# Performance work log

Hardware: AMD Instinct MI355X
Metric: run time of the kernel (lower is better)

The kernel has to match this reference:

```python
import jax, jax.numpy as jnp
import numpy as np

N = 25000   # nodes
E = 400000  # edges
F_IN = 128  # in_features
F_E = 16    # edge_features
C = 32      # channel_width
F_OUT = 1   # out_features
SLOPE = 0.01  # torch LeakyReLU default negative_slope


def leaky_relu(x):
    return jnp.where(x >= 0, x, SLOPE * x)


def setup_inputs() -> dict:
    key = jax.random.key(0)
    ks = jax.random.split(key, 12)
    x = jax.random.normal(ks[0], (N, F_IN), dtype=jnp.float32)
    edge_index = jax.random.randint(ks[1], (2, E), 0, N, dtype=jnp.int64)
    edge_attr = jax.random.normal(ks[2], (E, F_E), dtype=jnp.float32)
    # parameters (scaled like kaiming-ish fan-in init)
    W_in = jax.random.normal(ks[3], (F_IN, C), dtype=jnp.float32) / np.sqrt(F_IN)
    b_in = jnp.zeros((C,), dtype=jnp.float32)
    W_edge = jax.random.normal(ks[4], (F_E, C * C), dtype=jnp.float32) / np.sqrt(F_E)
    b_edge = jnp.zeros((C * C,), dtype=jnp.float32)
    W_root = jax.random.normal(ks[5], (C, C), dtype=jnp.float32) / np.sqrt(C)
    b_conv = jnp.zeros((C,), dtype=jnp.float32)
    W_out = jax.random.normal(ks[6], (C, F_OUT), dtype=jnp.float32) / np.sqrt(C)
    b_out = jnp.zeros((F_OUT,), dtype=jnp.float32)
    return {
        "x": x, "edge_index": edge_index, "edge_attr": edge_attr,
        "W_in": W_in, "b_in": b_in, "W_edge": W_edge, "b_edge": b_edge,
        "W_root": W_root, "b_conv": b_conv, "W_out": W_out, "b_out": b_out,
    }


def reference(x, edge_index, edge_attr, W_in, b_in, W_edge, b_edge,
              W_root, b_conv, W_out, b_out):
    # input projection (dropout = identity in eval mode)
    h = leaky_relu(x @ W_in + b_in)                       # [N, C]

    # NNConv layer (gnn_depth = 1):
    # per-edge weight matrix from edge_nn: Linear + LeakyReLU
    We = leaky_relu(edge_attr @ W_edge + b_edge)          # [E, C*C]
    We = We.reshape(E, C, C)                              # [E, C, C]
    src, dst = edge_index[0], edge_index[1]               # PyG: j=source, i=target
    # gather source node features, per-edge matvec, scatter-add to targets
    msg = jnp.einsum('ec,eco->eo', h[src], We)            # [E, C]
    aggr = jax.ops.segment_sum(msg, dst, num_segments=N)  # [N, C]
    h = aggr + h @ W_root + b_conv                        # root weight + bias
    h = leaky_relu(h)

    return h @ W_out + b_out                              # [N, F_OUT]
```

## Files before the change

### kernel.cpp

```cpp
#include <hip/hip_runtime.h>

#define NN 25000
#define EE 400000
#define FIN 128
#define FE 16
#define CH 32
#define SLOPE 0.01f
#define PROJ_BLOCKS 391
#define AUX_BLOCKS 32
#define WROW 24
#define WTP_SHORTS (1024 * WROW)
#define NTILES (EE / 128)
#define PBLK 1024

typedef __attribute__((ext_vector_type(8))) short bf16x8;
typedef __attribute__((ext_vector_type(4))) float f32x4;

__device__ __forceinline__ float lrelu(float v) { return fmaxf(v, SLOPE * v); }

__device__ __forceinline__ f32x4 lrelu4(f32x4 v) {
    f32x4 s = v * SLOPE;
#if __has_builtin(__builtin_elementwise_max)
    return __builtin_elementwise_max(v, s);
#else
    f32x4 r;
    r[0] = fmaxf(v[0], s[0]); r[1] = fmaxf(v[1], s[1]);
    r[2] = fmaxf(v[2], s[2]); r[3] = fmaxf(v[3], s[3]);
    return r;
#endif
}

__device__ __forceinline__ short f2bf(float f) {
    union { float f; unsigned u; } v; v.f = f;
    unsigned r = (v.u + 0x7fffu + ((v.u >> 16) & 1u)) >> 16;
    return (short)r;
}

__global__ void __launch_bounds__(256)
k_pre(const float* __restrict__ x, const float* __restrict__ W_in,
      const float* __restrict__ b_in, const float* __restrict__ W_edge,
      const float* __restrict__ b_edge,
      float* __restrict__ h, float* __restrict__ aggr, short* __restrict__ WtP) {
    __shared__ short Wt1[CH * 136];
    int tid = threadIdx.x;

    if (blockIdx.x >= PROJ_BLOCKS) {
        int ab = blockIdx.x - PROJ_BLOCKS;
        if (ab < 4) {
            int co = ab * 256 + tid;
            short row[WROW] __attribute__((aligned(16)));
#pragma unroll
            for (int k = 0; k < 16; k++) row[k] = f2bf(W_edge[k * 1024 + co]);
            row[16] = f2bf(b_edge[co]);
#pragma unroll
            for (int k = 17; k < WROW; k++) row[k] = 0;
            uint4* dstp = (uint4*)(WtP + co * WROW);
            int p0 = co % 3;
            int p1 = p0 + 1; if (p1 == 3) p1 = 0;
            int p2 = p1 + 1; if (p2 == 3) p2 = 0;
            dstp[p0] = ((uint4*)row)[0];
            dstp[p1] = ((uint4*)row)[1];
            dstp[p2] = ((uint4*)row)[2];
        } else {
            int t = (ab - 4) * 256 + tid;
            float4 z = make_float4(0.f, 0.f, 0.f, 0.f);
            for (int i = t; i < NN * CH / 4; i += (AUX_BLOCKS - 4) * 256)
                ((float4*)aggr)[i] = z;
        }
        return;
    }

#pragma unroll
    for (int i = 0; i < 16; i++) {
        int id = tid + 256 * i;
        int k = id >> 5, c = id & 31;
        Wt1[c * 136 + k] = f2bf(W_in[id]);
    }
    __syncthreads();

    int wave = tid >> 6, lane = tid & 63;
    int n16 = lane & 15, quad = lane >> 4;
    int node0 = blockIdx.x * 64 + wave * 16;

    f32x4 D[2];
#pragma unroll
    for (int ch = 0; ch < 2; ch++) {
        float bb = b_in[ch * 16 + n16];
        D[ch] = (f32x4){bb, bb, bb, bb};
    }
    int arow = node0 + n16; if (arow >= NN) arow = NN - 1;
#pragma unroll
    for (int kb = 0; kb < 4; kb++) {
        const float4* xp = (const float4*)(x + (size_t)arow * FIN + kb * 32 + quad * 8);
        float4 xa = xp[0], xb = xp[1];
        bf16x8 A = (bf16x8){f2bf(xa.x), f2bf(xa.y), f2bf(xa.z), f2bf(xa.w),
                            f2bf(xb.x), f2bf(xb.y), f2bf(xb.z), f2bf(xb.w)};
#pragma unroll
        for (int ch = 0; ch < 2; ch++) {
            bf16x8 B = *(const bf16x8*)&Wt1[(ch * 16 + n16) * 136 + kb * 32 + quad * 8];
            D[ch] = __builtin_amdgcn_mfma_f32_16x16x32_bf16(A, B, D[ch], 0, 0, 0);
        }
    }
#pragma unroll
    for (int ch = 0; ch < 2; ch++)
#pragma unroll
        for (int r = 0; r < 4; r++) {
            int nn = node0 + quad * 4 + r;
            if (nn < NN) h[(size_t)nn * CH + ch * 16 + n16] = lrelu(D[ch][r]);
        }
}

__global__ void __launch_bounds__(256, 2)
k_edge(const short* __restrict__ WtP,
       const float* __restrict__ ea,
       const int* __restrict__ src,
       const int* __restrict__ dst,
       const float* __restrict__ h,
       float* __restrict__ aggr) {
    __shared__ short WtL[WTP_SHORTS];
    __shared__ float hsT[2][CH * 128];

    int tid = threadIdx.x;

#pragma unroll
    for (int j = 0; j < 12; j++) {
        int idx = tid + 256 * j;
        ((uint4*)WtL)[idx] = ((const uint4*)WtP)[idx];
    }

    int eH = tid >> 1, halfH = tid & 1;
    int wave = tid >> 6, lane = tid & 63;
    int n16 = lane & 15, quad = lane >> 4;
    int t0 = wave * 32, t1 = t0 + 16;

    int s0 = (quad == 3) ? 0 : quad;
    int rot = (s0 + n16) % 3;
    const short* Bb[3];
#pragma unroll
    for (int j = 0; j < 3; j++) {
        int p = rot + j; if (p >= 3) p -= 3;
        Bb[j] = WtL + n16 * WROW + p * 8;
    }

    struct PrefT {
        float hv[16];
        float4 e0a, e0b, e1a, e1b;
        int d[8];
    };
    PrefT Pa, Pb;

    auto PREF = [&](int tile, PrefT& P) {
        int base = tile * 128;
        int s = src[base + eH];
        const float4* hp = (const float4*)(h + (size_t)s * CH + halfH * 16);
        float4 v0 = hp[0], v1 = hp[1], v2 = hp[2], v3 = hp[3];
        *(float4*)&P.hv[0] = v0;  *(float4*)&P.hv[4] = v1;
        *(float4*)&P.hv[8] = v2;  *(float4*)&P.hv[12] = v3;
        if (quad < 2) {
            const float4* p0 = (const float4*)(ea + (size_t)(base + t0 + n16) * FE + quad * 8);
            P.e0a = p0[0]; P.e0b = p0[1];
            const float4* p1 = (const float4*)(ea + (size_t)(base + t1 + n16) * FE + quad * 8);
            P.e1a = p1[0]; P.e1b = p1[1];
        }
#pragma unroll
        for (int r = 0; r < 4; r++) {
            P.d[r]     = dst[base + t0 + quad * 4 + r];
            P.d[4 + r] = dst[base + t1 + quad * 4 + r];
        }
    };

    auto WRITE = [&](float* hbuf, PrefT& P) {
        float* hd = hbuf + halfH * (16 * 128) + eH;
#pragma unroll
        for (int j = 0; j < 16; j++) hd[j * 128] = P.hv[j];
    };

    auto COMPUTE = [&](const float* hbuf, PrefT& P) {
        bf16x8 A0 = (bf16x8){0,0,0,0,0,0,0,0}, A1 = A0;
        if (quad < 2) {
            A0 = (bf16x8){f2bf(P.e0a.x), f2bf(P.e0a.y), f2bf(P.e0a.z), f2bf(P.e0a.w),
                          f2bf(P.e0b.x), f2bf(P.e0b.y), f2bf(P.e0b.z), f2bf(P.e0b.w)};
            A1 = (bf16x8){f2bf(P.e1a.x), f2bf(P.e1a.y), f2bf(P.e1a.z), f2bf(P.e1a.w),
                          f2bf(P.e1b.x), f2bf(P.e1b.y), f2bf(P.e1b.z), f2bf(P.e1b.w)};
        } else if (quad == 2) {
            A0[0] = (short)0x3F80; A1[0] = (short)0x3F80;
        }

        f32x4 m0[2], m1[2];
        m0[0] = (f32x4){0,0,0,0}; m0[1] = m0[0]; m1[0] = m0[0]; m1[1] = m0[0];
        const f32x4 Z = (f32x4){0,0,0,0};
        const float* h0b = hbuf + t0 + quad * 4;
        const float* h1b = hbuf + t1 + quad * 4;

#pragma unroll
        for (int c = 0; c < 32; c++) {
            f32x4 hc0 = *(const f32x4*)(h0b + c * 128);
            f32x4 hc1 = *(const f32x4*)(h1b + c * 128);
#pragma unroll
            for (int oh = 0; oh < 2; oh++) {
                int cb = c * 2 + oh;
                bf16x8 B = *(const bf16x8*)(Bb[cb % 3] + cb * (16 * WROW));
                f32x4 D0 = __builtin_amdgcn_mfma_f32_16x16x32_bf16(A0, B, Z, 0, 0, 0);
                f32x4 D1 = __builtin_amdgcn_mfma_f32_16x16x32_bf16(A1, B, Z, 0, 0, 0);
                m0[oh] += hc0 * lrelu4(D0);
                m1[oh] += hc1 * lrelu4(D1);
            }
        }

#pragma unroll
        for (int r = 0; r < 4; r++) {
#pragma unroll
            for (int oh = 0; oh < 2; oh++) {
                unsafeAtomicAdd(&aggr[(size_t)P.d[r]     * CH + oh * 16 + n16], m0[oh][r]);
                unsafeAtomicAdd(&aggr[(size_t)P.d[4 + r] * CH + oh * 16 + n16], m1[oh][r]);
            }
        }
    };

    int tile = blockIdx.x;
    PREF(tile, Pa);
    while (true) {
        WRITE(&hsT[0][0], Pa);
        __syncthreads();
        int nt = tile + PBLK;
        bool more = (nt < NTILES);
        if (more) PREF(nt, Pb);
        COMPUTE(&hsT[0][0], Pa);
        if (!more) break;
        tile = nt;

        WRITE(&hsT[1][0], Pb);
        __syncthreads();
        nt = tile + PBLK;
        more = (nt < NTILES);
        if (more) PREF(nt, Pa);
        COMPUTE(&hsT[1][0], Pb);
        if (!more) break;
        tile = nt;
    }
}

__global__ void __launch_bounds__(256)
k_node(const float* __restrict__ aggr,
       const float* __restrict__ h,
       const float* __restrict__ W_root,
       const float* __restrict__ b_conv,
       const float* __restrict__ W_out,
       const float* __restrict__ b_out,
       float* __restrict__ out) {
    __shared__ short WrB[CH * 40];
    __shared__ float WoS[CH];
    int tid = threadIdx.x;
    if (tid < 128) {
        int o = tid >> 2, c0 = (tid & 3) * 8;
        short tmp[8] __attribute__((aligned(16)));
#pragma unroll
        for (int j = 0; j < 8; j++) tmp[j] = f2bf(W_root[(c0 + j) * CH + o]);
        *(bf16x8*)&WrB[o * 40 + c0] = *(bf16x8*)tmp;
    } else if (tid < 160) {
        WoS[tid - 128] = W_out[tid - 128];
    }
    __syncthreads();

    int wave = tid >> 6, lane = tid & 63;
    int n16 = lane & 15, quad = lane >> 4;
    int node0 = blockIdx.x * 64 + wave * 16;

    int arow = node0 + n16; if (arow >= NN) arow = NN - 1;
    const float4* hp = (const float4*)(h + (size_t)arow * CH + quad * 8);
    float4 ha = hp[0], hb = hp[1];
    bf16x8 A = (bf16x8){f2bf(ha.x), f2bf(ha.y), f2bf(ha.z), f2bf(ha.w),
                        f2bf(hb.x), f2bf(hb.y), f2bf(hb.z), f2bf(hb.w)};
    float bc0 = b_conv[n16], bc1 = b_conv[16 + n16];
    f32x4 C0, C1;
#pragma unroll
    for (int r = 0; r < 4; r++) {
        int nr = node0 + quad * 4 + r; int cr = (nr < NN) ? nr : NN - 1;
        C0[r] = aggr[(size_t)cr * CH + n16] + bc0;
        C1[r] = aggr[(size_t)cr * CH + 16 + n16] + bc1;
    }
    bf16x8 B0 = *(const bf16x8*)&WrB[n16 * 40 + quad * 8];
    bf16x8 B1 = *(const bf16x8*)&WrB[(16 + n16) * 40 + quad * 8];
    f32x4 D0 = __builtin_amdgcn_mfma_f32_16x16x32_bf16(A, B0, C0, 0, 0, 0);
    f32x4 D1 = __builtin_amdgcn_mfma_f32_16x16x32_bf16(A, B1, C1, 0, 0, 0);

    float w0 = WoS[n16], w1 = WoS[16 + n16];
    f32x4 p;
#pragma unroll
    for (int r = 0; r < 4; r++)
        p[r] = lrelu(D0[r]) * w0 + lrelu(D1[r]) * w1;
#pragma unroll
    for (int mk = 1; mk < 16; mk <<= 1) {
#pragma unroll
        for (int r = 0; r < 4; r++) p[r] += __shfl_xor(p[r], mk, 64);
    }
    if (n16 == 0) {
        float bo = b_out[0];
#pragma unroll
        for (int r = 0; r < 4; r++) {
            int nr = node0 + quad * 4 + r;
            if (nr < NN) out[nr] = p[r] + bo;
        }
    }
}

extern "C" void kernel_launch(void* const* d_in, const int* in_sizes, int n_in,
                              void* d_out, int out_size, void* d_ws, size_t ws_size,
                              hipStream_t stream) {
    const float* x      = (const float*)d_in[0];
    const int*   ei     = (const int*)d_in[1];
    const float* ea     = (const float*)d_in[2];
    const float* W_in   = (const float*)d_in[3];
    const float* b_in   = (const float*)d_in[4];
    const float* W_edge = (const float*)d_in[5];
    const float* b_edge = (const float*)d_in[6];
    const float* W_root = (const float*)d_in[7];
    const float* b_conv = (const float*)d_in[8];
    const float* W_out  = (const float*)d_in[9];
    const float* b_out  = (const float*)d_in[10];
    float* out  = (float*)d_out;
    float* h    = (float*)d_ws;
    float* aggr = h + (size_t)NN * CH;
    short* WtP  = (short*)(aggr + (size_t)NN * CH);

    k_pre<<<PROJ_BLOCKS + AUX_BLOCKS, 256, 0, stream>>>(x, W_in, b_in, W_edge, b_edge,
                                                        h, aggr, WtP);
    k_edge<<<PBLK, 256, 0, stream>>>(WtP, ea, ei, ei + EE, h, aggr);
    k_node<<<PROJ_BLOCKS, 256, 0, stream>>>(aggr, h, W_root, b_conv, W_out, b_out, out);
}
```

Measured before the change: 163.6 us.

## Move edge bias to MFMA accumulator init and compact swizzled W_edge LDS layout

The edge-network bias no longer rides in the MFMA K dimension as a padded 24-short row with rotated placement. It is loaded as fp32 into LDS and fed in as the MFMA C accumulator. The bf16 weight table shrinks to 16 shorts per output with an XOR swizzle to avoid bank conflicts. This cuts LDS footprint, drops the three-way rotating pointer arithmetic, and keeps the bias in full precision. The h staging goes from double-buffered to a single buffer with an extra barrier, and the grid drops from 1024 to 768 blocks, which may cost some overlap between loads and compute.

```diff
diff --git a/kernel.cpp b/kernel.cpp
--- a/kernel.cpp
+++ b/kernel.cpp
@@ -8,10 +8,10 @@
 #define SLOPE 0.01f
 #define PROJ_BLOCKS 391
 #define AUX_BLOCKS 32
-#define WROW 24
-#define WTP_SHORTS (1024 * WROW)
-#define NTILES (EE / 128)
-#define PBLK 1024
+#define W16_SHORTS (1024 * 16)
+#define EPT 128
+#define NT (EE / EPT)
+#define PBLK 768
 
 typedef __attribute__((ext_vector_type(8))) short bf16x8;
 typedef __attribute__((ext_vector_type(4))) float f32x4;
@@ -36,11 +36,16 @@
     return (short)r;
 }
 
+__device__ __forceinline__ bf16x8 cvt8(const float4& a, const float4& b) {
+    return (bf16x8){f2bf(a.x), f2bf(a.y), f2bf(a.z), f2bf(a.w),
+                    f2bf(b.x), f2bf(b.y), f2bf(b.z), f2bf(b.w)};
+}
+
 __global__ void __launch_bounds__(256)
 k_pre(const float* __restrict__ x, const float* __restrict__ W_in,
       const float* __restrict__ b_in, const float* __restrict__ W_edge,
       const float* __restrict__ b_edge,
-      float* __restrict__ h, float* __restrict__ aggr, short* __restrict__ WtP) {
+      float* __restrict__ h, float* __restrict__ aggr, short* __restrict__ WtP16) {
     __shared__ short Wt1[CH * 136];
     int tid = threadIdx.x;
 
@@ -48,19 +53,11 @@
         int ab = blockIdx.x - PROJ_BLOCKS;
         if (ab < 4) {
             int co = ab * 256 + tid;
-            short row[WROW] __attribute__((aligned(16)));
+            short row[16] __attribute__((aligned(16)));
 #pragma unroll
             for (int k = 0; k < 16; k++) row[k] = f2bf(W_edge[k * 1024 + co]);
-            row[16] = f2bf(b_edge[co]);
-#pragma unroll
-            for (int k = 17; k < WROW; k++) row[k] = 0;
-            uint4* dstp = (uint4*)(WtP + co * WROW);
-            int p0 = co % 3;
-            int p1 = p0 + 1; if (p1 == 3) p1 = 0;
-            int p2 = p1 + 1; if (p2 == 3) p2 = 0;
-            dstp[p0] = ((uint4*)row)[0];
-            dstp[p1] = ((uint4*)row)[1];
-            dstp[p2] = ((uint4*)row)[2];
+            uint4* dstp = (uint4*)(WtP16 + co * 16);
+            dstp[0] = ((uint4*)row)[0]; dstp[1] = ((uint4*)row)[1];
         } else {
             int t = (ab - 4) * 256 + tid;
             float4 z = make_float4(0.f, 0.f, 0.f, 0.f);
@@ -93,8 +90,7 @@
     for (int kb = 0; kb < 4; kb++) {
         const float4* xp = (const float4*)(x + (size_t)arow * FIN + kb * 32 + quad * 8);
         float4 xa = xp[0], xb = xp[1];
-        bf16x8 A = (bf16x8){f2bf(xa.x), f2bf(xa.y), f2bf(xa.z), f2bf(xa.w),
-                            f2bf(xb.x), f2bf(xb.y), f2bf(xb.z), f2bf(xb.w)};
+        bf16x8 A = cvt8(xa, xb);
 #pragma unroll
         for (int ch = 0; ch < 2; ch++) {
             bf16x8 B = *(const bf16x8*)&Wt1[(ch * 16 + n16) * 136 + kb * 32 + quad * 8];
@@ -111,36 +107,41 @@
 }
 
 __global__ void __launch_bounds__(256, 2)
-k_edge(const short* __restrict__ WtP,
+k_edge(const short* __restrict__ WtP16,
        const float* __restrict__ ea,
        const int* __restrict__ src,
        const int* __restrict__ dst,
        const float* __restrict__ h,
-       float* __restrict__ aggr) {
-    __shared__ short WtL[WTP_SHORTS];
-    __shared__ float hsT[2][CH * 128];
+       float* __restrict__ aggr,
+       const float* __restrict__ b_edge) {
+    __shared__ short W16[W16_SHORTS];
+    __shared__ float biasF[1024];
+    __shared__ float hsT[CH * EPT];
 
     int tid = threadIdx.x;
 
 #pragma unroll
-    for (int j = 0; j < 12; j++) {
+    for (int j = 0; j < 9; j++) {
         int idx = tid + 256 * j;
-        ((uint4*)WtL)[idx] = ((const uint4*)WtP)[idx];
-    }
-
-    int eH = tid >> 1, halfH = tid & 1;
-    int wave = tid >> 6, lane = tid & 63;
-    int n16 = lane & 15, quad = lane >> 4;
-    int t0 = wave * 32, t1 = t0 + 16;
-
-    int s0 = (quad == 3) ? 0 : quad;
-    int rot = (s0 + n16) % 3;
-    const short* Bb[3];
-#pragma unroll
-    for (int j = 0; j < 3; j++) {
-        int p = rot + j; if (p >= 3) p -= 3;
-        Bb[j] = WtL + n16 * WROW + p * 8;
-    }
+        if (idx < 2048) {
+            int co = idx >> 1, s = idx & 1;
+            int p = (co << 1) | (s ^ ((co >> 2) & 1));
+            ((uint4*)W16)[p] = ((const uint4*)WtP16)[idx];
+        } else if (idx < 2304) {
+            ((uint4*)biasF)[idx - 2048] = ((const uint4*)b_edge)[idx - 2048];
+        }
+    }
+
+    const int lane = tid & 63;
+    const int wave = tid >> 6;
+    const int n16 = lane & 15, quad = lane >> 4;
+    const int t0 = wave * 32, t1 = t0 + 16;
+    const int eH = tid >> 1, halfH = tid & 1;
+
+    const int qeff = (quad & 1) ^ ((n16 >> 2) & 1);
+    const short* Bbase = W16 + n16 * 16 + qeff * 8;
+    const float* h0b = hsT + t0 + quad * 4;
+    const float* h1b = hsT + t1 + quad * 4;
 
     struct PrefT {
         float hv[16];
@@ -150,7 +151,7 @@
     PrefT Pa, Pb;
 
     auto PREF = [&](int tile, PrefT& P) {
-        int base = tile * 128;
+        int base = tile * EPT;
         int s = src[base + eH];
         const float4* hp = (const float4*)(h + (size_t)s * CH + halfH * 16);
         float4 v0 = hp[0], v1 = hp[1], v2 = hp[2], v3 = hp[3];
@@ -169,41 +170,40 @@
         }
     };
 
-    auto WRITE = [&](float* hbuf, PrefT& P) {
-        float* hd = hbuf + halfH * (16 * 128) + eH;
-#pragma unroll
-        for (int j = 0; j < 16; j++) hd[j * 128] = P.hv[j];
+    auto WRITE = [&](PrefT& P) {
+        float* hd = hsT + halfH * (16 * EPT) + eH;
+#pragma unroll
+        for (int j = 0; j < 16; j++) hd[j * EPT] = P.hv[j];
     };
 
-    auto COMPUTE = [&](const float* hbuf, PrefT& P) {
+    auto COMPUTE = [&](PrefT& P) {
         bf16x8 A0 = (bf16x8){0,0,0,0,0,0,0,0}, A1 = A0;
-        if (quad < 2) {
-            A0 = (bf16x8){f2bf(P.e0a.x), f2bf(P.e0a.y), f2bf(P.e0a.z), f2bf(P.e0a.w),
-                          f2bf(P.e0b.x), f2bf(P.e0b.y), f2bf(P.e0b.z), f2bf(P.e0b.w)};
-            A1 = (bf16x8){f2bf(P.e1a.x), f2bf(P.e1a.y), f2bf(P.e1a.z), f2bf(P.e1a.w),
-                          f2bf(P.e1b.x), f2bf(P.e1b.y), f2bf(P.e1b.z), f2bf(P.e1b.w)};
-        } else if (quad == 2) {
-            A0[0] = (short)0x3F80; A1[0] = (short)0x3F80;
-        }
+        if (quad < 2) { A0 = cvt8(P.e0a, P.e0b); A1 = cvt8(P.e1a, P.e1b); }
 
         f32x4 m0[2], m1[2];
         m0[0] = (f32x4){0,0,0,0}; m0[1] = m0[0]; m1[0] = m0[0]; m1[1] = m0[0];
-        const f32x4 Z = (f32x4){0,0,0,0};
-        const float* h0b = hbuf + t0 + quad * 4;
-        const float* h1b = hbuf + t1 + quad * 4;
 
 #pragma unroll
         for (int c = 0; c < 32; c++) {
-            f32x4 hc0 = *(const f32x4*)(h0b + c * 128);
-            f32x4 hc1 = *(const f32x4*)(h1b + c * 128);
-#pragma unroll
-            for (int oh = 0; oh < 2; oh++) {
-                int cb = c * 2 + oh;
-                bf16x8 B = *(const bf16x8*)(Bb[cb % 3] + cb * (16 * WROW));
-                f32x4 D0 = __builtin_amdgcn_mfma_f32_16x16x32_bf16(A0, B, Z, 0, 0, 0);
-                f32x4 D1 = __builtin_amdgcn_mfma_f32_16x16x32_bf16(A1, B, Z, 0, 0, 0);
-                m0[oh] += hc0 * lrelu4(D0);
-                m1[oh] += hc1 * lrelu4(D1);
+            f32x4 hc0 = *(const f32x4*)(h0b + c * EPT);
+            f32x4 hc1 = *(const f32x4*)(h1b + c * EPT);
+            float b0 = biasF[32 * c + n16];
+            float b1 = biasF[32 * c + 16 + n16];
+            f32x4 Cb0 = (f32x4){b0, b0, b0, b0};
+            f32x4 Cb1 = (f32x4){b1, b1, b1, b1};
+            {
+                bf16x8 B = *(const bf16x8*)(Bbase + (2 * c) * 256);
+                f32x4 D0 = __builtin_amdgcn_mfma_f32_16x16x32_bf16(A0, B, Cb0, 0, 0, 0);
+                f32x4 D1 = __builtin_amdgcn_mfma_f32_16x16x32_bf16(A1, B, Cb0, 0, 0, 0);
+                m0[0] += lrelu4(D0) * hc0;
+                m1[0] += lrelu4(D1) * hc1;
+            }
+            {
+                bf16x8 B = *(const bf16x8*)(Bbase + (2 * c + 1) * 256);
+                f32x4 D0 = __builtin_amdgcn_mfma_f32_16x16x32_bf16(A0, B, Cb1, 0, 0, 0);
+                f32x4 D1 = __builtin_amdgcn_mfma_f32_16x16x32_bf16(A1, B, Cb1, 0, 0, 0);
+                m0[1] += lrelu4(D0) * hc0;
+                m1[1] += lrelu4(D1) * hc1;
             }
         }
 
@@ -217,26 +217,28 @@
         }
     };
 
-    int tile = blockIdx.x;
-    PREF(tile, Pa);
+    int T = blockIdx.x;
+    PREF(T, Pa);
     while (true) {
-        WRITE(&hsT[0][0], Pa);
         __syncthreads();
-        int nt = tile + PBLK;
-        bool more = (nt < NTILES);
+        WRITE(Pa);
+        __syncthreads();
+        int nt = T + PBLK;
+        bool more = (nt < NT);
         if (more) PREF(nt, Pb);
-        COMPUTE(&hsT[0][0], Pa);
+        COMPUTE(Pa);
         if (!more) break;
-        tile = nt;
-
-        WRITE(&hsT[1][0], Pb);
+        T = nt;
+
         __syncthreads();
-        nt = tile + PBLK;
-        more = (nt < NTILES);
+        WRITE(Pb);
+        __syncthreads();
+        nt = T + PBLK;
+        more = (nt < NT);
         if (more) PREF(nt, Pa);
-        COMPUTE(&hsT[1][0], Pb);
+        COMPUTE(Pb);
         if (!more) break;
-        tile = nt;
+        T = nt;
     }
 }
 
@@ -269,8 +271,7 @@
     int arow = node0 + n16; if (arow >= NN) arow = NN - 1;
     const float4* hp = (const float4*)(h + (size_t)arow * CH + quad * 8);
     float4 ha = hp[0], hb = hp[1];
-    bf16x8 A = (bf16x8){f2bf(ha.x), f2bf(ha.y), f2bf(ha.z), f2bf(ha.w),
-                        f2bf(hb.x), f2bf(hb.y), f2bf(hb.z), f2bf(hb.w)};
+    bf16x8 A = cvt8(ha, hb);
     float bc0 = b_conv[n16], bc1 = b_conv[16 + n16];
     f32x4 C0, C1;
 #pragma unroll
@@ -321,10 +322,10 @@
     float* out  = (float*)d_out;
     float* h    = (float*)d_ws;
     float* aggr = h + (size_t)NN * CH;
-    short* WtP  = (short*)(aggr + (size_t)NN * CH);
+    short* WtP16 = (short*)(aggr + (size_t)NN * CH);
 
     k_pre<<<PROJ_BLOCKS + AUX_BLOCKS, 256, 0, stream>>>(x, W_in, b_in, W_edge, b_edge,
-                                                        h, aggr, WtP);
-    k_edge<<<PBLK, 256, 0, stream>>>(WtP, ea, ei, ei + EE, h, aggr);
+                                                        h, aggr, WtP16);
+    k_edge<<<PBLK, 256, 0, stream>>>(WtP16, ea, ei, ei + EE, h, aggr, b_edge);
     k_node<<<PROJ_BLOCKS, 256, 0, stream>>>(aggr, h, W_root, b_conv, W_out, b_out, out);
 }
```

New measurement: 170.2 us. +4.0%, slower.
